# Optimization experiments

Measured on AMD Instinct MI355X. Metric: run time of the kernel, lower is better.

The kernel has to match this reference:

```python
import jax, jax.numpy as jnp
import numpy as np
from jax import lax

NF = 64
DG = 8          # deformable groups
K = 3
K2 = K * K
B, H, W = 4, 128, 128


def lrelu(x):
    return jnp.where(x >= 0, x, 0.1 * x)


def conv3(x, w, b):
    # 3x3, stride 1, pad 1 conv in NCHW/OIHW
    y = lax.conv_general_dilated(x, w, (1, 1), 'SAME',
                                 dimension_numbers=('NCHW', 'OIHW', 'NCHW'))
    return y + b[None, :, None, None]


def mod_deform_conv(x, offset, mask, w, b):
    """Modulated deformable conv v2 (3x3, stride 1, pad 1, dil 1, groups=1).
    x: [B,C,H,W]; offset: [B, DG*2*K2, H, W] (per group: [k2, (y,x)]);
    mask: [B, DG*K2, H, W] (already sigmoided); w: [C,C,3,3]; b: [C].
    """
    Bc, C, Hh, Ww = x.shape
    Cper = C // DG
    off = offset.reshape(Bc, DG, K2, 2, Hh, Ww)
    # base grid + kernel taps (pad=1 -> taps in {-1,0,1})
    ky, kx = jnp.meshgrid(jnp.arange(K) - 1, jnp.arange(K) - 1, indexing='ij')
    ky = ky.reshape(K2).astype(x.dtype)
    kx = kx.reshape(K2).astype(x.dtype)
    hs = jnp.arange(Hh, dtype=x.dtype)
    ws = jnp.arange(Ww, dtype=x.dtype)
    # sampling positions [B, DG, K2, H, W]
    py = hs[None, None, None, :, None] + ky[None, None, :, None, None] + off[:, :, :, 0]
    px = ws[None, None, None, None, :] + kx[None, None, :, None, None] + off[:, :, :, 1]

    y0 = jnp.floor(py).astype(jnp.int32)
    x0 = jnp.floor(px).astype(jnp.int32)
    ly = py - y0
    lx = px - x0

    xg = x.reshape(Bc, DG, Cper, Hh * Ww)

    def gather(yi, xi, wgt):
        valid = (yi >= 0) & (yi < Hh) & (xi >= 0) & (xi < Ww)
        idx = jnp.clip(yi, 0, Hh - 1) * Ww + jnp.clip(xi, 0, Ww - 1)
        idxf = idx.reshape(Bc, DG, 1, K2 * Hh * Ww)
        v = jnp.take_along_axis(xg, idxf, axis=-1).reshape(Bc, DG, Cper, K2, Hh, Ww)
        return v * (wgt * valid)[:, :, None]

    sampled = (gather(y0,     x0,     (1 - ly) * (1 - lx))
             + gather(y0,     x0 + 1, (1 - ly) * lx)
             + gather(y0 + 1, x0,     ly * (1 - lx))
             + gather(y0 + 1, x0 + 1, ly * lx))
    sampled = sampled * mask.reshape(Bc, DG, 1, K2, Hh, Ww)
    cols = sampled.reshape(Bc, C, K2, Hh, Ww)            # im2col columns
    out = jnp.einsum('bikhw,oik->bohw', cols, w.reshape(C, C, K2))
    return out + b[None, :, None, None]


def dcn_pack(feat, offset_feat, w_om, b_om, w_dcn, b_dcn):
    om = conv3(offset_feat, w_om, b_om)                  # [B, DG*3*K2, H, W]
    o1, o2, m = jnp.split(om, 3, axis=1)
    offset = jnp.concatenate([o1, o2], axis=1)           # [B, DG*2*K2, H, W]
    mask = jax.nn.sigmoid(m)                             # [B, DG*K2, H, W]
    return mod_deform_conv(feat, offset, mask, w_dcn, b_dcn)


def setup_inputs() -> dict:
    key = jax.random.key(0)
    ks = jax.random.split(key, 16)
    f32 = jnp.float32

    def wconv(k, cout, cin, scale=0.05):
        return scale * jax.random.normal(k, (cout, cin, 3, 3), dtype=f32)

    inp = {
        'fea_l':     jax.random.normal(ks[0], (B, NF, H, W), dtype=f32),
        'ref_fea_l': jax.random.normal(ks[1], (B, NF, H, W), dtype=f32),
        'w_off_fea1': wconv(ks[2], NF, NF * 2), 'b_off_fea1': jnp.zeros((NF,), f32),
        'w_off_fea2': wconv(ks[3], NF, NF),     'b_off_fea2': jnp.zeros((NF,), f32),
        'w_off_ref1': wconv(ks[4], NF, NF * 2), 'b_off_ref1': jnp.zeros((NF,), f32),
        'w_off_ref2': wconv(ks[5], NF, NF),     'b_off_ref2': jnp.zeros((NF,), f32),
        # conv_offset_mask: NF -> DG*3*K2 = 216, small init so offsets are modest
        'w_dcn_om': wconv(ks[6], DG * 3 * K2, NF, scale=0.01),
        'b_dcn_om': jnp.zeros((DG * 3 * K2,), f32),
        'w_dcn': wconv(ks[7], NF, NF), 'b_dcn': jnp.zeros((NF,), f32),
        'w_fuse1': wconv(ks[8], NF, NF * 2), 'b_fuse1': jnp.zeros((NF,), f32),
        'w_fuse2': wconv(ks[9], NF, NF),     'b_fuse2': jnp.zeros((NF,), f32),
    }
    return inp


def reference(fea_l, ref_fea_l,
              w_off_fea1, b_off_fea1, w_off_fea2, b_off_fea2,
              w_off_ref1, b_off_ref1, w_off_ref2, b_off_ref2,
              w_dcn_om, b_dcn_om, w_dcn, b_dcn,
              w_fuse1, b_fuse1, w_fuse2, b_fuse2):
    # offset branch for fea_l
    of = jnp.concatenate([fea_l, ref_fea_l], axis=1)
    of = lrelu(conv3(of, w_off_fea1, b_off_fea1))
    of = lrelu(conv3(of, w_off_fea2, b_off_fea2))
    deform_fea = lrelu(dcn_pack(fea_l, of, w_dcn_om, b_dcn_om, w_dcn, b_dcn))
    # offset branch for ref_fea_l (shared dcnpack weights)
    orr = jnp.concatenate([ref_fea_l, fea_l], axis=1)
    orr = lrelu(conv3(orr, w_off_ref1, b_off_ref1))
    orr = lrelu(conv3(orr, w_off_ref2, b_off_ref2))
    deform_ref = lrelu(dcn_pack(ref_fea_l, orr, w_dcn_om, b_dcn_om, w_dcn, b_dcn))
    # fusion
    cat = jnp.concatenate([deform_fea, deform_ref], axis=1)
    out = lrelu(conv3(cat, w_fuse1, b_fuse1))
    out = lrelu(conv3(out, w_fuse2, b_fuse2))
    return out
```

## Files before the change

kernel.cpp:

```cpp
#include <hip/hip_runtime.h>
#include <hip/hip_fp16.h>
#include <math.h>

#define HH 128
#define WW 128
#define PLANE (HH*WW)
#define BB 4

typedef _Float16 f16x8 __attribute__((ext_vector_type(8)));
typedef _Float16 f16x4 __attribute__((ext_vector_type(4)));
typedef float f32x4 __attribute__((ext_vector_type(4)));

__device__ __forceinline__ float lrelu(float v) { return v >= 0.f ? v : 0.1f * v; }

__device__ __forceinline__ uint32_t pack2h(float a, float b) {
    return (uint32_t)__half_as_ushort(__float2half(b)) << 16 |
           (uint32_t)__half_as_ushort(__float2half(a));
}

__global__ __launch_bounds__(256)
void convert_all_kernel(const float* __restrict__ fea, const float* __restrict__ ref,
                        __half* __restrict__ G0, __half* __restrict__ G1)
{
    const int j = blockIdx.x >> 8;
    const float* in = j ? ref : fea;
    __half* out     = j ? G1 : G0;
    int pix = (blockIdx.x & 255) * 256 + threadIdx.x;
    int b = pix >> 14;
    int p = pix & 16383;
    const float* src = in + (size_t)b * 64 * PLANE + p;
    uint32_t buf[32];
#pragma unroll
    for (int c = 0; c < 64; c += 2)
        buf[c >> 1] = pack2h(src[(size_t)c * PLANE], src[(size_t)(c + 1) * PLANE]);
#pragma unroll
    for (int g = 0; g < 8; ++g) {
        uint4* dst = (uint4*)(out + ((size_t)(b * 8 + g) * PLANE + p) * 8);
        *dst = make_uint4(buf[4*g], buf[4*g+1], buf[4*g+2], buf[4*g+3]);
    }
}

__device__ __forceinline__ void repack_w16_body(const float* __restrict__ src,
                                                __half* __restrict__ dst,
                                                int Cout, int Cin, int OPAD, int idx)
{
    int total = Cin * 9 * OPAD;
    if (idx >= total) return;
    int cp   = idx & 31;
    int o    = (idx >> 5) % OPAD;
    int rest = idx / (32 * OPAD);
    int tap  = rest % 9;
    int cc   = rest / 9;
    int c = cc * 32 + cp;
    float v = (o < Cout) ? src[((size_t)o * Cin + c) * 9 + tap] : 0.f;
    dst[idx] = __float2half(v);
}

__device__ __forceinline__ void repack_dcn_body(const float* __restrict__ w,
                                                __half* __restrict__ wr, int idx)
{
    if (idx >= 18 * 64 * 32) return;
    int k  = idx & 31;
    int o  = (idx >> 5) & 63;
    int cc = idx >> 11;
    int tl = k >> 3, c = k & 7;
    int gk = cc * 4 + tl;
    int g = gk / 9, k2 = gk - g * 9;
    wr[idx] = __float2half(w[((size_t)o * 64 + g * 8 + c) * 9 + k2]);
}

__global__ __launch_bounds__(256)
void repack_all_kernel(const float* w_of1, const float* w_or1, const float* w_of2,
                       const float* w_or2, const float* w_om,  const float* w_fu1,
                       const float* w_fu2, const float* w_dcn,
                       __half* W0, __half* W1, __half* W2, __half* W3,
                       __half* W4, __half* W5, __half* W6, __half* W7h)
{
    const int bx = blockIdx.x;
    const int t  = threadIdx.x;
    if      (bx <  288) repack_w16_body(w_of1, W0,  64, 128,  64, (bx       ) * 256 + t);
    else if (bx <  576) repack_w16_body(w_or1, W1,  64, 128,  64, (bx -  288) * 256 + t);
    else if (bx <  720) repack_w16_body(w_of2, W2,  64,  64,  64, (bx -  576) * 256 + t);
    else if (bx <  864) repack_w16_body(w_or2, W3,  64,  64,  64, (bx -  720) * 256 + t);
    else if (bx < 1440) repack_w16_body(w_om,  W4, 216,  64, 256, (bx -  864) * 256 + t);
    else if (bx < 1728) repack_w16_body(w_fu1, W5,  64, 128,  64, (bx - 1440) * 256 + t);
    else if (bx < 1872) repack_w16_body(w_fu2, W6,  64,  64,  64, (bx - 1728) * 256 + t);
    else                repack_dcn_body(w_dcn, W7h,               (bx - 1872) * 256 + t);
}

template<int KG, int CHUNKS, int OUTMODE, bool GIN, bool SWZ>
__global__ __launch_bounds__(256, 4)
void conv_mfma_kernel(const __half* __restrict__ x0a, const __half* __restrict__ x1a,
                      const __half* __restrict__ x0b, const __half* __restrict__ x1b,
                      const __half* __restrict__ wa,  const __half* __restrict__ wb,
                      const float* __restrict__ ba,   const float* __restrict__ bb,
                      void* __restrict__ outa, void* __restrict__ outb,
                      int CoutReal)
{
    constexpr int OPAD = CHUNKS * 64;
    const int tid  = threadIdx.x;
    const int lane = tid & 63;
    const int wv   = tid >> 6;
    const int p16  = lane & 15;
    const int q    = lane >> 4;

    int job, b, chunk, tx0, ty0;
    if (SWZ) {
        job = blockIdx.x >> 2;  b = blockIdx.x & 3;
        chunk = (CHUNKS > 1) ? (blockIdx.z >> 3) : 0;
        ty0 = ((CHUNKS > 1) ? (blockIdx.z & 7) : blockIdx.z) * 16;
        tx0 = blockIdx.y * 16;
    } else {
        const int zz = blockIdx.z;
        job = zz / (BB * CHUNKS);
        const int rem = zz % (BB * CHUNKS);
        chunk = rem / BB;  b = rem % BB;
        tx0 = blockIdx.x * 16;  ty0 = blockIdx.y * 16;
    }
    const int oc0 = chunk * 64;

    const __half* x0  = job ? x0b : x0a;
    const __half* x1  = job ? x1b : x1a;
    const __half* wr  = job ? wb  : wa;
    const float* bias = job ? bb  : ba;
    void* outp        = job ? outb : outa;

    __shared__ __align__(16) __half act[18 * 18 * 40];

    f32x4 acc[4][4];
#pragma unroll
    for (int mt = 0; mt < 4; ++mt)
#pragma unroll
        for (int nt = 0; nt < 4; ++nt)
            acc[mt][nt] = (f32x4)(0.f);

#pragma unroll 1
    for (int kg = 0; kg < KG; ++kg) {
        {
            const __half* src = (KG == 4 && kg >= 2) ? x1 : x0;
            const int csel = (KG == 4) ? (kg & 1) : kg;
#pragma unroll
            for (int i = 0; i < 6; ++i) {
                int t = tid + i * 256;
                if (t < 1296) {
                    int pix = t >> 2, qq = t & 3;
                    int ry = pix / 18, cx = pix - ry * 18;
                    int y = ty0 + ry - 1, x = tx0 + cx - 1;
                    uint4 v = make_uint4(0, 0, 0, 0);
                    if ((unsigned)y < HH && (unsigned)x < WW) {
                        if (GIN)
                            v = *(const uint4*)(src + ((size_t)(b * 8 + csel * 4 + qq) * PLANE
                                                + (y * WW + x)) * 8);
                        else
                            v = *(const uint4*)(src + ((size_t)((b * HH + y) * WW + x)) * 64
                                                + csel * 32 + qq * 8);
                    }
                    *(uint4*)(&act[pix * 40 + qq * 8]) = v;
                }
            }
        }
        __syncthreads();

#pragma unroll 3
        for (int tap = 0; tap < 9; ++tap) {
            const int step = kg * 9 + tap;
            f16x8 af[4];
#pragma unroll
            for (int mt = 0; mt < 4; ++mt)
                af[mt] = *(const f16x8*)(wr
                    + ((size_t)(step * OPAD + oc0 + mt * 16 + p16)) * 32 + q * 8);
            const int dy = tap / 3, dx = tap % 3;
#pragma unroll
            for (int nt = 0; nt < 4; ++nt) {
                int ry = 4 * wv + nt + dy;
                int cx = p16 + dx;
                f16x8 bf = *(const f16x8*)(&act[(ry * 18 + cx) * 40 + q * 8]);
#pragma unroll
                for (int mt = 0; mt < 4; ++mt)
                    acc[mt][nt] = __builtin_amdgcn_mfma_f32_16x16x32_f16(
                        af[mt], bf, acc[mt][nt], 0, 0, 0);
            }
        }
        __syncthreads();
    }

    float bv[4][4];
#pragma unroll
    for (int mt = 0; mt < 4; ++mt)
#pragma unroll
        for (int r = 0; r < 4; ++r) {
            int o = oc0 + mt * 16 + q * 4 + r;
            bv[mt][r] = (o < CoutReal) ? bias[o] : 0.f;
        }

    const int xg = tx0 + p16;
#pragma unroll
    for (int nt = 0; nt < 4; ++nt) {
        int yg = ty0 + 4 * wv + nt;
        if (OUTMODE == 0) {
            __half* op = (__half*)outp + ((size_t)((b * HH + yg) * WW + xg)) * 64;
#pragma unroll
            for (int mt = 0; mt < 4; ++mt) {
                float v0 = lrelu(acc[mt][nt][0] + bv[mt][0]);
                float v1 = lrelu(acc[mt][nt][1] + bv[mt][1]);
                float v2 = lrelu(acc[mt][nt][2] + bv[mt][2]);
                float v3 = lrelu(acc[mt][nt][3] + bv[mt][3]);
                *(uint2*)(op + mt * 16 + q * 4) = make_uint2(pack2h(v0, v1), pack2h(v2, v3));
            }
        } else if (OUTMODE == 1) {
            __half* op = (__half*)outp
                       + ((size_t)(chunk * BB + b) * PLANE + yg * WW + xg) * 64;
#pragma unroll
            for (int mt = 0; mt < 4; ++mt) {
                int o = oc0 + mt * 16 + q * 4;
                if (o + 3 < 216) {
                    float v0 = acc[mt][nt][0] + bv[mt][0];
                    float v1 = acc[mt][nt][1] + bv[mt][1];
                    float v2 = acc[mt][nt][2] + bv[mt][2];
                    float v3 = acc[mt][nt][3] + bv[mt][3];
                    *(uint2*)(op + mt * 16 + q * 4) = make_uint2(pack2h(v0, v1), pack2h(v2, v3));
                }
            }
        } else {
            float* op = (float*)outp + ((size_t)(b * 64) * HH) * WW + yg * WW + xg;
#pragma unroll
            for (int mt = 0; mt < 4; ++mt)
#pragma unroll
                for (int r = 0; r < 4; ++r) {
                    int o = mt * 16 + q * 4 + r;
                    op[(size_t)o * PLANE] = lrelu(acc[mt][nt][r] + bv[mt][r]);
                }
        }
    }
}

__global__ __launch_bounds__(512, 4)
void dcn_mfma_kernel(const __half* __restrict__ ga, const __half* __restrict__ gb,
                     const __half* __restrict__ oma, const __half* __restrict__ omb,
                     const __half* __restrict__ wr, const float* __restrict__ bias,
                     __half* __restrict__ outa, __half* __restrict__ outb)
{
    const int tid  = threadIdx.x;
    const int half = tid >> 8;
    const int t8   = tid & 255;
    const int lane = tid & 63;
    const int wv4  = (tid >> 6) & 3;
    const int p16  = lane & 15;
    const int q    = lane >> 4;
    const int job  = blockIdx.x >> 2;
    const int b    = blockIdx.x & 3;
    const int tx0  = blockIdx.y * 16;
    const int ty0  = blockIdx.z * 16;

    const __half* G  = job ? gb : ga;
    const __half* om = job ? omb : oma;
    __half* out      = job ? outb : outa;

    const int xs = tx0 + (t8 & 15);
    const int ys = ty0 + (t8 >> 4);
    const int pxl = ys * WW + xs;

    __shared__ __align__(16) __half colbuf[2][256 * 40];

    f32x4 acc[4][4];
#pragma unroll
    for (int mt = 0; mt < 4; ++mt)
#pragma unroll
        for (int nt = 0; nt < 4; ++nt)
            acc[mt][nt] = (f32x4)(0.f);

#pragma unroll 1
    for (int i = 0; i < 9; ++i) {
        const int cc = half * 9 + i;

        const int ch_d = 72 * half + 8 * i;
        const int ch_m = 144 + 36 * half + 4 * i;
        f16x8 ddv = *(const f16x8*)(om + ((size_t)((ch_d >> 6) * BB + b) * PLANE + pxl) * 64
                                    + (ch_d & 63));
        f16x4 mkv = *(const f16x4*)(om + ((size_t)((ch_m >> 6) * BB + b) * PLANE + pxl) * 64
                                    + (ch_m & 63));

        f16x8 af[4];
#pragma unroll
        for (int mt = 0; mt < 4; ++mt)
            af[mt] = *(const f16x8*)(wr + ((size_t)(cc * 64 + mt * 16 + p16)) * 32 + q * 8);

#pragma unroll
        for (int tl = 0; tl < 4; ++tl) {
            int gk = cc * 4 + tl;
            int g  = gk / 9;
            int k2 = gk - g * 9;
            int kyi = k2 / 3, kxi = k2 - kyi * 3;

            float dyo = (float)ddv[2 * tl];
            float dxo = (float)ddv[2 * tl + 1];
            float mk  = 1.f / (1.f + expf(-(float)mkv[tl]));

            float py = (float)(ys + kyi - 1) + dyo;
            float px = (float)(xs + kxi - 1) + dxo;
            float fy = floorf(py), fx = floorf(px);
            int   y0 = (int)fy,    x0 = (int)fx;
            float ly = py - fy,    lx = px - fx;
            int   y1 = y0 + 1,     x1 = x0 + 1;

            float vy0 = (y0 >= 0 && y0 < HH) ? 1.f : 0.f;
            float vy1 = (y1 >= 0 && y1 < HH) ? 1.f : 0.f;
            float vx0 = (x0 >= 0 && x0 < WW) ? 1.f : 0.f;
            float vx1 = (x1 >= 0 && x1 < WW) ? 1.f : 0.f;

            _Float16 w00 = (_Float16)((1.f - ly) * (1.f - lx) * vy0 * vx0 * mk);
            _Float16 w01 = (_Float16)((1.f - ly) * lx         * vy0 * vx1 * mk);
            _Float16 w10 = (_Float16)(ly         * (1.f - lx) * vy1 * vx0 * mk);
            _Float16 w11 = (_Float16)(ly         * lx         * vy1 * vx1 * mk);

            int cy0 = min(max(y0, 0), HH - 1);
            int cy1 = min(max(y1, 0), HH - 1);
            int cx0 = min(max(x0, 0), WW - 1);
            int cx1 = min(max(x1, 0), WW - 1);
            const __half* gp = G + (size_t)(b * 8 + g) * PLANE * 8;
            f16x8 c00 = *(const f16x8*)(gp + (size_t)(cy0 * WW + cx0) * 8);
            f16x8 c01 = *(const f16x8*)(gp + (size_t)(cy0 * WW + cx1) * 8);
            f16x8 c10 = *(const f16x8*)(gp + (size_t)(cy1 * WW + cx0) * 8);
            f16x8 c11 = *(const f16x8*)(gp + (size_t)(cy1 * WW + cx1) * 8);

            f16x8 pv = c00 * w00 + c01 * w01 + c10 * w10 + c11 * w11;
            *(f16x8*)(&colbuf[half][t8 * 40 + tl * 8]) = pv;
        }

#pragma unroll
        for (int nt = 0; nt < 4; ++nt) {
            f16x8 bf = *(const f16x8*)(&colbuf[half][(wv4 * 64 + nt * 16 + p16) * 40 + q * 8]);
#pragma unroll
            for (int mt = 0; mt < 4; ++mt)
                acc[mt][nt] = __builtin_amdgcn_mfma_f32_16x16x32_f16(
                    af[mt], bf, acc[mt][nt], 0, 0, 0);
        }
    }

    __syncthreads();

    float* red = (float*)&colbuf[0][0];
#pragma unroll
    for (int mt = 0; mt < 4; ++mt) {
        if (half == 1) {
#pragma unroll
            for (int nt = 0; nt < 4; ++nt) {
                int pxi = wv4 * 64 + nt * 16 + p16;
                *(f32x4*)(&red[pxi * 17 + q * 4]) = acc[mt][nt];
            }
        }
        __syncthreads();
        if (half == 0) {
#pragma unroll
            for (int nt = 0; nt < 4; ++nt) {
                int pxi = wv4 * 64 + nt * 16 + p16;
                f32x4 v = *(const f32x4*)(&red[pxi * 17 + q * 4]);
                acc[mt][nt] += v;
            }
        }
        __syncthreads();
    }

    if (half == 0) {
        const int xg = tx0 + p16;
#pragma unroll
        for (int nt = 0; nt < 4; ++nt) {
            int yg = ty0 + 4 * wv4 + nt;
            __half* op = out + ((size_t)((b * HH + yg) * WW + xg)) * 64;
#pragma unroll
            for (int mt = 0; mt < 4; ++mt) {
                int o = mt * 16 + q * 4;
                float v0 = lrelu(acc[mt][nt][0] + bias[o]);
                float v1 = lrelu(acc[mt][nt][1] + bias[o + 1]);
                float v2 = lrelu(acc[mt][nt][2] + bias[o + 2]);
                float v3 = lrelu(acc[mt][nt][3] + bias[o + 3]);
                *(uint2*)(op + o) = make_uint2(pack2h(v0, v1), pack2h(v2, v3));
            }
        }
    }
}

extern "C" void kernel_launch(void* const* d_in, const int* in_sizes, int n_in,
                              void* d_out, int out_size, void* d_ws, size_t ws_size,
                              hipStream_t stream) {
    const float* fea   = (const float*)d_in[0];
    const float* ref   = (const float*)d_in[1];
    const float* w_of1 = (const float*)d_in[2];
    const float* b_of1 = (const float*)d_in[3];
    const float* w_of2 = (const float*)d_in[4];
    const float* b_of2 = (const float*)d_in[5];
    const float* w_or1 = (const float*)d_in[6];
    const float* b_or1 = (const float*)d_in[7];
    const float* w_or2 = (const float*)d_in[8];
    const float* b_or2 = (const float*)d_in[9];
    const float* w_om  = (const float*)d_in[10];
    const float* b_om  = (const float*)d_in[11];
    const float* w_dcn = (const float*)d_in[12];
    const float* b_dcn = (const float*)d_in[13];
    const float* w_fu1 = (const float*)d_in[14];
    const float* b_fu1 = (const float*)d_in[15];
    const float* w_fu2 = (const float*)d_in[16];
    const float* b_fu2 = (const float*)d_in[17];

    char* ws = (char*)d_ws;
    constexpr size_t SLOT = (size_t)BB * PLANE * 64 * 2;
    constexpr size_t OMSZ = 4 * SLOT;
    __half* W0  = (__half*)(ws);
    __half* W1  = (__half*)(ws + 147456);
    __half* W2  = (__half*)(ws + 294912);
    __half* W3  = (__half*)(ws + 368640);
    __half* W4  = (__half*)(ws + 442368);
    __half* W5  = (__half*)(ws + 737280);
    __half* W6  = (__half*)(ws + 884736);
    __half* W7h = (__half*)(ws + 958464);
    __half* G0  = (__half*)(ws + 1048576);
    __half* G1  = (__half*)(ws + 1048576 + SLOT);
    __half* Y   = (__half*)(ws + 1048576 + 2 * SLOT);
    __half* Z   = (__half*)(ws + 1048576 + 3 * SLOT);
    char*  OMa_ = ws + 1048576 + 4 * SLOT;
    char*  OMb_ = OMa_ + OMSZ;
    __half* OMa = (__half*)OMa_;
    __half* OMb = (__half*)OMb_;
    __half* X2  = (__half*)OMa_;
    __half* X3  = (__half*)(OMa_ + SLOT);
    __half* D0  = Y;
    __half* D1  = Z;
    __half* F   = G0;

    dim3 blk(256, 1, 1);

    repack_all_kernel<<<2016, blk, 0, stream>>>(
        w_of1, w_or1, w_of2, w_or2, w_om, w_fu1, w_fu2, w_dcn,
        W0, W1, W2, W3, W4, W5, W6, W7h);
    convert_all_kernel<<<512, blk, 0, stream>>>(fea, ref, G0, G1);

    conv_mfma_kernel<4, 1, 0, true, true><<<dim3(8, 8, 8), blk, 0, stream>>>(
        G0, G1, G1, G0, W0, W1, b_of1, b_or1, X2, X3, 64);
    conv_mfma_kernel<2, 1, 0, false, false><<<dim3(8, 8, 8), blk, 0, stream>>>(
        X2, X2, X3, X3, W2, W3, b_of2, b_or2, Y, Z, 64);
    conv_mfma_kernel<2, 4, 1, false, true><<<dim3(8, 8, 32), blk, 0, stream>>>(
        Y, Y, Z, Z, W4, W4, b_om, b_om, OMa, OMb, 216);
    dcn_mfma_kernel<<<dim3(8, 8, 8), dim3(512, 1, 1), 0, stream>>>(
        G0, G1, OMa, OMb, W7h, b_dcn, D0, D1);
    conv_mfma_kernel<4, 1, 0, false, false><<<dim3(8, 8, 4), blk, 0, stream>>>(
        D0, D1, D0, D1, W5, W5, b_fu1, b_fu1, F, F, 64);
    conv_mfma_kernel<2, 1, 2, false, false><<<dim3(8, 8, 4), blk, 0, stream>>>(
        F, F, F, F, W6, W6, b_fu2, b_fu2, d_out, d_out, 64);

    (void)in_sizes; (void)n_in; (void)out_size; (void)ws_size;
}
```

Baseline: 284.4 us.

## Split DCN K-reduction four ways over 16x8 tiles to double block count

The deformable-conv kernel now processes 16x8 pixel tiles with four 128-thread groups, each handling a quarter of the 18 channel chunks, instead of 16x16 tiles split across two halves. The grid doubles in the z dimension, giving more blocks for the GPU to spread across its compute units, and the cross-group reduction through shared memory now sums three partial buffers. Sigmoid also switches to the fast __expf intrinsic. In exchange, each tile costs more reduction traffic and synchronization, and the uneven 4/5-chunk split leaves some groups idle for part of the loop.

```diff
diff --git a/kernel.cpp b/kernel.cpp
--- a/kernel.cpp
+++ b/kernel.cpp
@@ -241,26 +241,26 @@
                      __half* __restrict__ outa, __half* __restrict__ outb)
 {
     const int tid  = threadIdx.x;
-    const int half = tid >> 8;
-    const int t8   = tid & 255;
+    const int qtr  = tid >> 7;
+    const int t7   = tid & 127;
     const int lane = tid & 63;
-    const int wv4  = (tid >> 6) & 3;
+    const int wv2  = (tid >> 6) & 1;
     const int p16  = lane & 15;
     const int q    = lane >> 4;
     const int job  = blockIdx.x >> 2;
     const int b    = blockIdx.x & 3;
     const int tx0  = blockIdx.y * 16;
-    const int ty0  = blockIdx.z * 16;
+    const int ty0  = blockIdx.z * 8;
 
     const __half* G  = job ? gb : ga;
     const __half* om = job ? omb : oma;
     __half* out      = job ? outb : outa;
 
-    const int xs = tx0 + (t8 & 15);
-    const int ys = ty0 + (t8 >> 4);
+    const int xs = tx0 + (t7 & 15);
+    const int ys = ty0 + (t7 >> 4);
     const int pxl = ys * WW + xs;
 
-    __shared__ __align__(16) __half colbuf[2][256 * 40];
+    __shared__ __align__(16) __half colbuf[4][128 * 40];
 
     f32x4 acc[4][4];
 #pragma unroll
@@ -269,12 +269,13 @@
         for (int nt = 0; nt < 4; ++nt)
             acc[mt][nt] = (f32x4)(0.f);
 
+    const int cc0 = (qtr * 18) >> 2;
+    const int cc1 = ((qtr + 1) * 18) >> 2;
+
 #pragma unroll 1
-    for (int i = 0; i < 9; ++i) {
-        const int cc = half * 9 + i;
-
-        const int ch_d = 72 * half + 8 * i;
-        const int ch_m = 144 + 36 * half + 4 * i;
+    for (int cc = cc0; cc < cc1; ++cc) {
+        const int ch_d = 8 * cc;
+        const int ch_m = 144 + 4 * cc;
         f16x8 ddv = *(const f16x8*)(om + ((size_t)((ch_d >> 6) * BB + b) * PLANE + pxl) * 64
                                     + (ch_d & 63));
         f16x4 mkv = *(const f16x4*)(om + ((size_t)((ch_m >> 6) * BB + b) * PLANE + pxl) * 64
@@ -294,7 +295,7 @@
 
             float dyo = (float)ddv[2 * tl];
             float dxo = (float)ddv[2 * tl + 1];
-            float mk  = 1.f / (1.f + expf(-(float)mkv[tl]));
+            float mk  = 1.f / (1.f + __expf(-(float)mkv[tl]));
 
             float py = (float)(ys + kyi - 1) + dyo;
             float px = (float)(xs + kxi - 1) + dxo;
@@ -324,12 +325,12 @@
             f16x8 c11 = *(const f16x8*)(gp + (size_t)(cy1 * WW + cx1) * 8);
 
             f16x8 pv = c00 * w00 + c01 * w01 + c10 * w10 + c11 * w11;
-            *(f16x8*)(&colbuf[half][t8 * 40 + tl * 8]) = pv;
+            *(f16x8*)(&colbuf[qtr][t7 * 40 + tl * 8]) = pv;
         }
 
 #pragma unroll
         for (int nt = 0; nt < 4; ++nt) {
-            f16x8 bf = *(const f16x8*)(&colbuf[half][(wv4 * 64 + nt * 16 + p16) * 40 + q * 8]);
+            f16x8 bf = *(const f16x8*)(&colbuf[qtr][(wv2 * 64 + nt * 16 + p16) * 40 + q * 8]);
 #pragma unroll
             for (int mt = 0; mt < 4; ++mt)
                 acc[mt][nt] = __builtin_amdgcn_mfma_f32_16x16x32_f16(
@@ -342,30 +343,31 @@
     float* red = (float*)&colbuf[0][0];
 #pragma unroll
     for (int mt = 0; mt < 4; ++mt) {
-        if (half == 1) {
+        if (qtr != 0) {
 #pragma unroll
             for (int nt = 0; nt < 4; ++nt) {
-                int pxi = wv4 * 64 + nt * 16 + p16;
-                *(f32x4*)(&red[pxi * 17 + q * 4]) = acc[mt][nt];
+                int pxi = wv2 * 64 + nt * 16 + p16;
+                *(f32x4*)(&red[((qtr - 1) * 128 + pxi) * 17 + q * 4]) = acc[mt][nt];
             }
         }
         __syncthreads();
-        if (half == 0) {
+        if (qtr == 0) {
 #pragma unroll
             for (int nt = 0; nt < 4; ++nt) {
-                int pxi = wv4 * 64 + nt * 16 + p16;
-                f32x4 v = *(const f32x4*)(&red[pxi * 17 + q * 4]);
-                acc[mt][nt] += v;
+                int pxi = wv2 * 64 + nt * 16 + p16;
+                acc[mt][nt] += *(const f32x4*)(&red[(pxi) * 17 + q * 4]);
+                acc[mt][nt] += *(const f32x4*)(&red[(128 + pxi) * 17 + q * 4]);
+                acc[mt][nt] += *(const f32x4*)(&red[(256 + pxi) * 17 + q * 4]);
             }
         }
         __syncthreads();
     }
 
-    if (half == 0) {
+    if (qtr == 0) {
         const int xg = tx0 + p16;
 #pragma unroll
         for (int nt = 0; nt < 4; ++nt) {
-            int yg = ty0 + 4 * wv4 + nt;
+            int yg = ty0 + 4 * wv2 + nt;
             __half* op = out + ((size_t)((b * HH + yg) * WW + xg)) * 64;
 #pragma unroll
             for (int mt = 0; mt < 4; ++mt) {
@@ -440,7 +442,7 @@
         X2, X2, X3, X3, W2, W3, b_of2, b_or2, Y, Z, 64);
     conv_mfma_kernel<2, 4, 1, false, true><<<dim3(8, 8, 32), blk, 0, stream>>>(
         Y, Y, Z, Z, W4, W4, b_om, b_om, OMa, OMb, 216);
-    dcn_mfma_kernel<<<dim3(8, 8, 8), dim3(512, 1, 1), 0, stream>>>(
+    dcn_mfma_kernel<<<dim3(8, 8, 16), dim3(512, 1, 1), 0, stream>>>(
         G0, G1, OMa, OMb, W7h, b_dcn, D0, D1);
     conv_mfma_kernel<4, 1, 0, false, false><<<dim3(8, 8, 4), blk, 0, stream>>>(
         D0, D1, D0, D1, W5, W5, b_fu1, b_fu1, F, F, 64);
```

New measurement: 274.5 us. -3.5%, faster.
